# Performance work log

Measured on AMD Instinct MI355X. Metric: run time of the kernel, lower is better.

The kernel has to match this reference:

```python
import jax, jax.numpy as jnp
import numpy as np

EPS = 1e-5

def setup_inputs() -> dict:
    key = jax.random.key(0)
    k1, k2, k3, k4, k5 = jax.random.split(key, 5)
    x = jax.random.normal(k1, (2048, 64, 768), dtype=jnp.float32)
    ln_w = jnp.ones((768,), dtype=jnp.float32)
    ln_b = jnp.zeros((768,), dtype=jnp.float32)
    # nn.Linear default init: U(-1/sqrt(in), 1/sqrt(in))
    bound = 1.0 / np.sqrt(768.0)
    W = jax.random.uniform(k2, (64, 768), dtype=jnp.float32, minval=-bound, maxval=bound)
    b = jax.random.uniform(k3, (64,), dtype=jnp.float32, minval=-bound, maxval=bound)
    return {"x": x, "ln_w": ln_w, "ln_b": ln_b, "W": W, "b": b}

def reference(x, ln_w, ln_b, W, b):
    B = x.shape[0]
    # LayerNorm over last dim (768)
    mu = jnp.mean(x, axis=-1, keepdims=True)
    var = jnp.mean(jnp.square(x - mu), axis=-1, keepdims=True)
    xn = (x - mu) * jax.lax.rsqrt(var + EPS) * ln_w + ln_b
    # Linear 768 -> 64, then SiLU
    y = jnp.einsum('bch,oh->bco', xn, W) + b
    y = y * jax.nn.sigmoid(y)
    # unpatchify: [B,64,64] -> [B,8,8,4,4,4] -> permute(0,3,1,4,2,5) -> [B,4,32,32]
    y = y.reshape(B, 8, 8, 4, 4, 4)
    y = jnp.transpose(y, (0, 3, 1, 4, 2, 5))
    return y.reshape(B, 4, 32, 32)
```

## Files before the change

### kernel.cpp

```cpp
#include <hip/hip_runtime.h>
#include <hip/hip_bf16.h>
#include <cstdint>

typedef __attribute__((ext_vector_type(8))) short s16x8;
typedef __attribute__((ext_vector_type(4))) float f32x4;

union CV2 { __hip_bfloat162 h; uint32_t u; };

__global__ void prep_kernel(const float* __restrict__ W,
                            const float* __restrict__ lnw,
                            const float* __restrict__ lnb,
                            const float* __restrict__ bias,
                            __hip_bfloat16* __restrict__ Wb,
                            float* __restrict__ Ssum,
                            float* __restrict__ bp) {
    const int o = blockIdx.x;
    const int tid = threadIdx.x;
    float s = 0.f, bb = 0.f;
    for (int k = tid; k < 768; k += 256) {
        float wraw = W[o * 768 + k];
        float wv = lnw[k] * wraw;
        s += wv;
        bb += lnb[k] * wraw;
        int kk = k >> 5, rem = k & 31;
        int q = rem >> 3, j = rem & 7;
        int t = o >> 4, n = o & 15;
        int l = q * 16 + n;
        Wb[(kk * 4 + t) * 512 + l * 8 + j] = __float2bfloat16(wv);
    }
    __shared__ float rs[4], rb[4];
    for (int off = 32; off > 0; off >>= 1) {
        s  += __shfl_down(s, off);
        bb += __shfl_down(bb, off);
    }
    int wid = tid >> 6;
    if ((tid & 63) == 0) { rs[wid] = s; rb[wid] = bb; }
    __syncthreads();
    if (tid == 0) {
        Ssum[o] = rs[0] + rs[1] + rs[2] + rs[3];
        bp[o]   = bias[o] + rb[0] + rb[1] + rb[2] + rb[3];
    }
}

__global__ __launch_bounds__(256, 2) void fused_kernel(
        const float* __restrict__ x,
        const uint4* __restrict__ Wb4,
        const float* __restrict__ Ssum,
        const float* __restrict__ bp,
        float* __restrict__ out) {
    const int b   = blockIdx.x;
    const int tid = threadIdx.x;
    const int w   = tid >> 6;
    const int l   = tid & 63;
    const int q   = l >> 4;
    const int n   = l & 15;

    __shared__ __align__(16) char lds[2 * 17408 + 2 * 16384];

    const float* xb = x + (size_t)b * 49152;
    const int srow = tid >> 5;
    const int u    = tid & 31;

    float4 st[8];
    uint4  wst[4];

    #pragma unroll
    for (int j = 0; j < 8; j++)
        st[j] = *(const float4*)(xb + (j * 8 + srow) * 768 + u * 4);
    #pragma unroll
    for (int j = 0; j < 4; j++)
        wst[j] = Wb4[tid + j * 256];
    #pragma unroll
    for (int j = 0; j < 8; j++) {
        CV2 lo, hi;
        lo.h = __float22bfloat162_rn(make_float2(st[j].x, st[j].y));
        hi.h = __float22bfloat162_rn(make_float2(st[j].z, st[j].w));
        *(uint2*)(lds + (j * 8 + srow) * 272 + u * 8) = make_uint2(lo.u, hi.u);
    }
    #pragma unroll
    for (int j = 0; j < 4; j++)
        *(uint4*)(lds + 34816 + (tid + j * 256) * 16) = wst[j];

    #pragma unroll
    for (int j = 0; j < 8; j++)
        st[j] = *(const float4*)(xb + (j * 8 + srow) * 768 + 128 + u * 4);
    #pragma unroll
    for (int j = 0; j < 4; j++)
        wst[j] = Wb4[1024 + tid + j * 256];
    __syncthreads();

    f32x4 acc0 = {0.f, 0.f, 0.f, 0.f};
    f32x4 acc1 = acc0, acc2 = acc0, acc3 = acc0;
    float sum = 0.f, ssq = 0.f;

    #pragma unroll
    for (int c = 0; c < 6; c++) {
        const char* xbp = lds + (c & 1) * 17408 + (w * 16 + n) * 272 + q * 16;
        uint4 fr[4];
        #pragma unroll
        for (int s = 0; s < 4; s++) fr[s] = *(const uint4*)(xbp + s * 64);

        const char* wbp = lds + 34816 + (c & 1) * 16384 + l * 16;

        #pragma unroll
        for (int s = 0; s < 4; s++) {
            union { uint4 u4; unsigned short us[8]; } fu; fu.u4 = fr[s];
            #pragma unroll
            for (int j = 0; j < 8; j++) {
                float xv = __uint_as_float(((unsigned)fu.us[j]) << 16);
                sum += xv;
                ssq = fmaf(xv, xv, ssq);
            }
            uint4 wb0 = *(const uint4*)(wbp + (s * 4 + 0) * 1024);
            uint4 wb1 = *(const uint4*)(wbp + (s * 4 + 1) * 1024);
            uint4 wb2 = *(const uint4*)(wbp + (s * 4 + 2) * 1024);
            uint4 wb3 = *(const uint4*)(wbp + (s * 4 + 3) * 1024);
            s16x8 af = __builtin_bit_cast(s16x8, fr[s]);
            acc0 = __builtin_amdgcn_mfma_f32_16x16x32_bf16(
                       af, __builtin_bit_cast(s16x8, wb0), acc0, 0, 0, 0);
            acc1 = __builtin_amdgcn_mfma_f32_16x16x32_bf16(
                       af, __builtin_bit_cast(s16x8, wb1), acc1, 0, 0, 0);
            acc2 = __builtin_amdgcn_mfma_f32_16x16x32_bf16(
                       af, __builtin_bit_cast(s16x8, wb2), acc2, 0, 0, 0);
            acc3 = __builtin_amdgcn_mfma_f32_16x16x32_bf16(
                       af, __builtin_bit_cast(s16x8, wb3), acc3, 0, 0, 0);
        }

        if (c < 5) {
            char* xo = lds + ((c + 1) & 1) * 17408;
            char* wo = lds + 34816 + ((c + 1) & 1) * 16384;
            #pragma unroll
            for (int j = 0; j < 8; j++) {
                CV2 lo, hi;
                lo.h = __float22bfloat162_rn(make_float2(st[j].x, st[j].y));
                hi.h = __float22bfloat162_rn(make_float2(st[j].z, st[j].w));
                *(uint2*)(xo + (j * 8 + srow) * 272 + u * 8) =
                    make_uint2(lo.u, hi.u);
            }
            #pragma unroll
            for (int j = 0; j < 4; j++)
                *(uint4*)(wo + (tid + j * 256) * 16) = wst[j];
            if (c < 4) {
                #pragma unroll
                for (int j = 0; j < 8; j++)
                    st[j] = *(const float4*)(xb + (j * 8 + srow) * 768
                                             + (c + 2) * 128 + u * 4);
                #pragma unroll
                for (int j = 0; j < 4; j++)
                    wst[j] = Wb4[(c + 2) * 1024 + tid + j * 256];
            }
            __syncthreads();
        }
    }

    sum += __shfl_xor(sum, 16); sum += __shfl_xor(sum, 32);
    ssq += __shfl_xor(ssq, 16); ssq += __shfl_xor(ssq, 32);
    const float mu   = sum * (1.0f / 768.0f);
    const float rstd = rsqrtf(ssq * (1.0f / 768.0f) - mu * mu + 1e-5f);

    float St[4], Bt[4];
    #pragma unroll
    for (int t = 0; t < 4; t++) {
        St[t] = Ssum[t * 16 + n];
        Bt[t] = bp[t * 16 + n];
    }

    float* sout = (float*)lds;
    const int o2 = (n >> 2) & 3;
    const int o3 = n & 3;
    f32x4 va[4] = {acc0, acc1, acc2, acc3};
    #pragma unroll
    for (int r = 0; r < 4; r++) {
        float mu_r   = __shfl(mu,   q * 4 + r);
        float rstd_r = __shfl(rstd, q * 4 + r);
        int cc  = w * 16 + q * 4 + r;
        int c1i = cc >> 3, c2i = cc & 7;
        int base = (c1i * 4 + o2) * 32 + c2i * 4 + o3;
        #pragma unroll
        for (int t = 0; t < 4; t++) {
            float y = rstd_r * (va[t][r] - mu_r * St[t]) + Bt[t];
            y = y / (1.0f + __expf(-y));
            sout[t * 1024 + base] = y;
        }
    }
    __syncthreads();

    float* outp = out + (size_t)b * 4096;
    #pragma unroll
    for (int j = 0; j < 4; j++) {
        *(float4*)(outp + j * 1024 + tid * 4) =
            *(const float4*)(&sout[j * 1024 + tid * 4]);
    }
}

extern "C" void kernel_launch(void* const* d_in, const int* in_sizes, int n_in,
                              void* d_out, int out_size, void* d_ws, size_t ws_size,
                              hipStream_t stream) {
    const float* x    = (const float*)d_in[0];
    const float* lnw  = (const float*)d_in[1];
    const float* lnb  = (const float*)d_in[2];
    const float* W    = (const float*)d_in[3];
    const float* bias = (const float*)d_in[4];
    float* out = (float*)d_out;

    const int B = in_sizes[0] / (64 * 768);

    __hip_bfloat16* Wb = (__hip_bfloat16*)d_ws;
    float* Ssum = (float*)((char*)d_ws + 98304);
    float* bp   = (float*)((char*)d_ws + 98304 + 256);

    prep_kernel<<<64, 256, 0, stream>>>(W, lnw, lnb, bias, Wb, Ssum, bp);
    fused_kernel<<<B, 256, 0, stream>>>(x, (const uint4*)d_ws, Ssum, bp, out);
}
```

Before: 547.5 us.

## Load x and W fragments directly from global into registers, drop LDS staging

Removes the LDS double-buffer staging of x and W. Each lane now loads its own MFMA A-fragment from global memory as fp32, converts it to bf16 in registers, and computes LayerNorm statistics on the fp32 values. W fragments are read straight from global (L2-resident) per MFMA, and the next chunk of x is prefetched into registers one step ahead. This removes the block-wide barriers and cuts LDS use to the output buffer, and launch bounds are raised to 3 blocks per SM. The trade-off is less coalesced global loads of x (32-byte segments per lane per row), repeated global/L2 reads of W by every wave, and higher register pressure from the prefetch buffers.

```diff
diff --git a/kernel.cpp b/kernel.cpp
--- a/kernel.cpp
+++ b/kernel.cpp
@@ -42,7 +42,7 @@
     }
 }
 
-__global__ __launch_bounds__(256, 2) void fused_kernel(
+__global__ __launch_bounds__(256, 3) void fused_kernel(
         const float* __restrict__ x,
         const uint4* __restrict__ Wb4,
         const float* __restrict__ Ssum,
@@ -55,101 +55,72 @@
     const int q   = l >> 4;
     const int n   = l & 15;
 
-    __shared__ __align__(16) char lds[2 * 17408 + 2 * 16384];
+    __shared__ __align__(16) float sout[4096];
 
-    const float* xb = x + (size_t)b * 49152;
-    const int srow = tid >> 5;
-    const int u    = tid & 31;
-
-    float4 st[8];
-    uint4  wst[4];
-
-    #pragma unroll
-    for (int j = 0; j < 8; j++)
-        st[j] = *(const float4*)(xb + (j * 8 + srow) * 768 + u * 4);
-    #pragma unroll
-    for (int j = 0; j < 4; j++)
-        wst[j] = Wb4[tid + j * 256];
-    #pragma unroll
-    for (int j = 0; j < 8; j++) {
-        CV2 lo, hi;
-        lo.h = __float22bfloat162_rn(make_float2(st[j].x, st[j].y));
-        hi.h = __float22bfloat162_rn(make_float2(st[j].z, st[j].w));
-        *(uint2*)(lds + (j * 8 + srow) * 272 + u * 8) = make_uint2(lo.u, hi.u);
-    }
-    #pragma unroll
-    for (int j = 0; j < 4; j++)
-        *(uint4*)(lds + 34816 + (tid + j * 256) * 16) = wst[j];
-
-    #pragma unroll
-    for (int j = 0; j < 8; j++)
-        st[j] = *(const float4*)(xb + (j * 8 + srow) * 768 + 128 + u * 4);
-    #pragma unroll
-    for (int j = 0; j < 4; j++)
-        wst[j] = Wb4[1024 + tid + j * 256];
-    __syncthreads();
+    const float* xr = x + (size_t)b * 49152 + (w * 16 + n) * 768 + q * 8;
+    const uint4* Wl = Wb4 + l;
 
     f32x4 acc0 = {0.f, 0.f, 0.f, 0.f};
     f32x4 acc1 = acc0, acc2 = acc0, acc3 = acc0;
     float sum = 0.f, ssq = 0.f;
 
+    float4 cur[8], nxt[8];
+    #pragma unroll
+    for (int s = 0; s < 4; s++) {
+        cur[2 * s]     = *(const float4*)(xr + s * 32);
+        cur[2 * s + 1] = *(const float4*)(xr + s * 32 + 4);
+    }
+
     #pragma unroll
     for (int c = 0; c < 6; c++) {
-        const char* xbp = lds + (c & 1) * 17408 + (w * 16 + n) * 272 + q * 16;
-        uint4 fr[4];
+        s16x8 af[4];
         #pragma unroll
-        for (int s = 0; s < 4; s++) fr[s] = *(const uint4*)(xbp + s * 64);
+        for (int s = 0; s < 4; s++) {
+            float4 lo = cur[2 * s], hi = cur[2 * s + 1];
+            sum += lo.x; ssq = fmaf(lo.x, lo.x, ssq);
+            sum += lo.y; ssq = fmaf(lo.y, lo.y, ssq);
+            sum += lo.z; ssq = fmaf(lo.z, lo.z, ssq);
+            sum += lo.w; ssq = fmaf(lo.w, lo.w, ssq);
+            sum += hi.x; ssq = fmaf(hi.x, hi.x, ssq);
+            sum += hi.y; ssq = fmaf(hi.y, hi.y, ssq);
+            sum += hi.z; ssq = fmaf(hi.z, hi.z, ssq);
+            sum += hi.w; ssq = fmaf(hi.w, hi.w, ssq);
+            CV2 p0, p1, p2, p3;
+            p0.h = __float22bfloat162_rn(make_float2(lo.x, lo.y));
+            p1.h = __float22bfloat162_rn(make_float2(lo.z, lo.w));
+            p2.h = __float22bfloat162_rn(make_float2(hi.x, hi.y));
+            p3.h = __float22bfloat162_rn(make_float2(hi.z, hi.w));
+            af[s] = __builtin_bit_cast(s16x8,
+                        make_uint4(p0.u, p1.u, p2.u, p3.u));
+        }
 
-        const char* wbp = lds + 34816 + (c & 1) * 16384 + l * 16;
+        if (c < 5) {
+            #pragma unroll
+            for (int s = 0; s < 4; s++) {
+                nxt[2 * s]     = *(const float4*)(xr + (c + 1) * 128 + s * 32);
+                nxt[2 * s + 1] = *(const float4*)(xr + (c + 1) * 128 + s * 32 + 4);
+            }
+        }
 
         #pragma unroll
         for (int s = 0; s < 4; s++) {
-            union { uint4 u4; unsigned short us[8]; } fu; fu.u4 = fr[s];
-            #pragma unroll
-            for (int j = 0; j < 8; j++) {
-                float xv = __uint_as_float(((unsigned)fu.us[j]) << 16);
-                sum += xv;
-                ssq = fmaf(xv, xv, ssq);
-            }
-            uint4 wb0 = *(const uint4*)(wbp + (s * 4 + 0) * 1024);
-            uint4 wb1 = *(const uint4*)(wbp + (s * 4 + 1) * 1024);
-            uint4 wb2 = *(const uint4*)(wbp + (s * 4 + 2) * 1024);
-            uint4 wb3 = *(const uint4*)(wbp + (s * 4 + 3) * 1024);
-            s16x8 af = __builtin_bit_cast(s16x8, fr[s]);
+            uint4 wb0 = Wl[((c * 4 + s) * 4 + 0) * 64];
+            uint4 wb1 = Wl[((c * 4 + s) * 4 + 1) * 64];
+            uint4 wb2 = Wl[((c * 4 + s) * 4 + 2) * 64];
+            uint4 wb3 = Wl[((c * 4 + s) * 4 + 3) * 64];
             acc0 = __builtin_amdgcn_mfma_f32_16x16x32_bf16(
-                       af, __builtin_bit_cast(s16x8, wb0), acc0, 0, 0, 0);
+                       af[s], __builtin_bit_cast(s16x8, wb0), acc0, 0, 0, 0);
             acc1 = __builtin_amdgcn_mfma_f32_16x16x32_bf16(
-                       af, __builtin_bit_cast(s16x8, wb1), acc1, 0, 0, 0);
+                       af[s], __builtin_bit_cast(s16x8, wb1), acc1, 0, 0, 0);
             acc2 = __builtin_amdgcn_mfma_f32_16x16x32_bf16(
-                       af, __builtin_bit_cast(s16x8, wb2), acc2, 0, 0, 0);
+                       af[s], __builtin_bit_cast(s16x8, wb2), acc2, 0, 0, 0);
             acc3 = __builtin_amdgcn_mfma_f32_16x16x32_bf16(
-                       af, __builtin_bit_cast(s16x8, wb3), acc3, 0, 0, 0);
+                       af[s], __builtin_bit_cast(s16x8, wb3), acc3, 0, 0, 0);
         }
 
         if (c < 5) {
-            char* xo = lds + ((c + 1) & 1) * 17408;
-            char* wo = lds + 34816 + ((c + 1) & 1) * 16384;
             #pragma unroll
-            for (int j = 0; j < 8; j++) {
-                CV2 lo, hi;
-                lo.h = __float22bfloat162_rn(make_float2(st[j].x, st[j].y));
-                hi.h = __float22bfloat162_rn(make_float2(st[j].z, st[j].w));
-                *(uint2*)(xo + (j * 8 + srow) * 272 + u * 8) =
-                    make_uint2(lo.u, hi.u);
-            }
-            #pragma unroll
-            for (int j = 0; j < 4; j++)
-                *(uint4*)(wo + (tid + j * 256) * 16) = wst[j];
-            if (c < 4) {
-                #pragma unroll
-                for (int j = 0; j < 8; j++)
-                    st[j] = *(const float4*)(xb + (j * 8 + srow) * 768
-                                             + (c + 2) * 128 + u * 4);
-                #pragma unroll
-                for (int j = 0; j < 4; j++)
-                    wst[j] = Wb4[(c + 2) * 1024 + tid + j * 256];
-            }
-            __syncthreads();
+            for (int i = 0; i < 8; i++) cur[i] = nxt[i];
         }
     }
 
@@ -165,7 +136,6 @@
         Bt[t] = bp[t * 16 + n];
     }
 
-    float* sout = (float*)lds;
     const int o2 = (n >> 2) & 3;
     const int o3 = n & 3;
     f32x4 va[4] = {acc0, acc1, acc2, acc3};
```

After: 613.7 us. 1.12x slower.
